# Kernel optimization log

Hardware: AMD Instinct MI355X
Metric: run time of the kernel (lower is better)

Reference implementation:

```python
import jax, jax.numpy as jnp
import numpy as np

D = 1024
H = 16
DH = D // H
FF = 4096
EPS = 1e-5


def _layernorm(x, g, b):
    m = jnp.mean(x, axis=-1, keepdims=True)
    v = jnp.mean(jnp.square(x - m), axis=-1, keepdims=True)
    return (x - m) * jax.lax.rsqrt(v + EPS) * g + b


def setup_inputs() -> dict:
    key = jax.random.key(0)
    ks = jax.random.split(key, 24)
    B, S = 2, 2048
    s = 0.02
    inp = {
        "tokens": jax.random.normal(ks[0], (B, S, D), jnp.float32),
        "attention_bias": jax.random.normal(ks[1], (B, S, S, 3), jnp.float32),
        "metadata_compatibility": jax.random.normal(ks[2], (B, S, S), jnp.float32),
        "key_padding_mask": jnp.zeros((B, S), jnp.bool_),
        "ln1_g": jnp.ones((D,), jnp.float32),
        "ln1_b": jnp.zeros((D,), jnp.float32),
        "Wq": jax.random.normal(ks[3], (D, D), jnp.float32) * s,
        "bq": jnp.zeros((D,), jnp.float32),
        "Wk": jax.random.normal(ks[4], (D, D), jnp.float32) * s,
        "bk": jnp.zeros((D,), jnp.float32),
        "Wv": jax.random.normal(ks[5], (D, D), jnp.float32) * s,
        "bv": jnp.zeros((D,), jnp.float32),
        "Wo": jax.random.normal(ks[6], (D, D), jnp.float32) * s,
        "bo": jnp.zeros((D,), jnp.float32),
        "Ws": jax.random.normal(ks[7], (3, H), jnp.float32) * s,
        "bs": jnp.zeros((H,), jnp.float32),
        "Wm": jax.random.normal(ks[8], (1, H), jnp.float32) * s,
        "bm": jnp.zeros((H,), jnp.float32),
        "ln2_g": jnp.ones((D,), jnp.float32),
        "ln2_b": jnp.zeros((D,), jnp.float32),
        "W1": jax.random.normal(ks[9], (D, FF), jnp.float32) * s,
        "b1": jnp.zeros((FF,), jnp.float32),
        "W2": jax.random.normal(ks[10], (FF, D), jnp.float32) * s,
        "b2": jnp.zeros((D,), jnp.float32),
    }
    return inp


def reference(tokens, attention_bias, metadata_compatibility, key_padding_mask,
              ln1_g, ln1_b, Wq, bq, Wk, bk, Wv, bv, Wo, bo,
              Ws, bs, Wm, bm, ln2_g, ln2_b, W1, b1, W2, b2):
    B, S, _ = tokens.shape
    scale = DH ** -0.5
    n = _layernorm(tokens, ln1_g, ln1_b)
    # project and split heads: [B,S,H,DH]
    q = (n @ Wq + bq).reshape(B, S, H, DH)
    k = (n @ Wk + bk).reshape(B, S, H, DH)
    v = (n @ Wv + bv).reshape(B, S, H, DH)
    logits = jnp.einsum('bihd,bjhd->bhij', q, k) * scale  # [B,H,S,S]
    # structural bias: Linear(3->H) then permute to [B,H,S,S]
    logits = logits + jnp.einsum('bijc,ch->bhij', attention_bias, Ws) + bs[None, :, None, None]
    # metadata bias: Linear(1->H)
    logits = logits + metadata_compatibility[:, None, :, :] * Wm[0][None, :, None, None] + bm[None, :, None, None]
    logits = jnp.where(key_padding_mask[:, None, None, :], -1e9, logits)
    w = jax.nn.softmax(logits, axis=-1)
    attended = jnp.einsum('bhij,bjhd->bihd', w, v).reshape(B, S, D)
    x = tokens + (attended @ Wo + bo)
    h = _layernorm(x, ln2_g, ln2_b)
    ff = jax.nn.gelu(h @ W1 + b1, approximate=False) @ W2 + b2
    return x + ff
```

## Files before the change

### kernel.cpp

```cpp
#include <hip/hip_runtime.h>

#define S_LEN 2048
#define DMODEL 1024
#define NH 16
#define DH 64
#define FFDIM 4096

typedef __bf16 bf16x8 __attribute__((ext_vector_type(8)));
typedef float f32x4 __attribute__((ext_vector_type(4)));
typedef unsigned short ushort_t;

#define AS1 __attribute__((address_space(1)))
#define AS3 __attribute__((address_space(3)))

__device__ __forceinline__ void gll16(const void* g, void* l) {
  __builtin_amdgcn_global_load_lds((AS1 const void*)g, (AS3 void*)l, 16, 0, 0);
}

__device__ __forceinline__ unsigned short f2b(float f){
  unsigned u = __builtin_bit_cast(unsigned, f);
  u = (u + 0x7FFFu + ((u >> 16) & 1u)) >> 16;
  return (unsigned short)u;
}

__device__ __forceinline__ float b2f(unsigned short us){
  return __builtin_bit_cast(float, (unsigned)us << 16);
}

__device__ __forceinline__ float gelu_exact(float x){
  return 0.5f * x * (1.0f + erff(x * 0.70710678118654752f));
}

__device__ __forceinline__ f32x4 mfma16(bf16x8 a, bf16x8 b, f32x4 c){
  return __builtin_amdgcn_mfma_f32_16x16x32_bf16(a, b, c, 0, 0, 0);
}

__global__ __launch_bounds__(256) void tconv_kernel(
    const float* __restrict__ W, ushort_t* __restrict__ Wt, int K, int N)
{
  __shared__ float tile[32][33];
  int tx = threadIdx.x, ty = threadIdx.y;
  int n0 = blockIdx.x * 32, k0 = blockIdx.y * 32;
#pragma unroll
  for (int i = 0; i < 4; ++i)
    tile[ty + i*8][tx] = W[(size_t)(k0 + ty + i*8) * N + n0 + tx];
  __syncthreads();
#pragma unroll
  for (int i = 0; i < 4; ++i)
    Wt[(size_t)(n0 + ty + i*8) * K + k0 + tx] = f2b(tile[tx][ty + i*8]);
}

__global__ __launch_bounds__(256) void ln_kernel(
    const float* __restrict__ x, const float* __restrict__ g,
    const float* __restrict__ bt, ushort_t* __restrict__ out)
{
  int row = blockIdx.x;
  int t = threadIdx.x;
  const float4 v = *(const float4*)&x[(size_t)row * DMODEL + t * 4];
  float s = v.x + v.y + v.z + v.w;
  float s2 = v.x*v.x + v.y*v.y + v.z*v.z + v.w*v.w;
#pragma unroll
  for (int d = 1; d < 64; d <<= 1) {
    s  += __shfl_xor(s,  d, 64);
    s2 += __shfl_xor(s2, d, 64);
  }
  __shared__ float red[8];
  int w = t >> 6;
  if ((t & 63) == 0) { red[w] = s; red[4 + w] = s2; }
  __syncthreads();
  s  = red[0] + red[1] + red[2] + red[3];
  s2 = red[4] + red[5] + red[6] + red[7];
  float mean = s * (1.0f / DMODEL);
  float var  = s2 * (1.0f / DMODEL) - mean * mean;
  float rstd = rsqrtf(var + 1e-5f);
  float4 gg = *(const float4*)&g[t * 4];
  float4 bb = *(const float4*)&bt[t * 4];
  ushort4 o;
  o.x = f2b((v.x - mean) * rstd * gg.x + bb.x);
  o.y = f2b((v.y - mean) * rstd * gg.y + bb.y);
  o.z = f2b((v.z - mean) * rstd * gg.z + bb.z);
  o.w = f2b((v.w - mean) * rstd * gg.w + bb.w);
  *(ushort4*)&out[(size_t)row * DMODEL + t * 4] = o;
}

__global__ __launch_bounds__(256) void bias_head_kernel(
    const float* __restrict__ ab, const float* __restrict__ mc,
    const unsigned char* __restrict__ kp,
    const float* __restrict__ Ws, const float* __restrict__ bs,
    const float* __restrict__ Wm, const float* __restrict__ bm,
    ushort_t* __restrict__ bp)
{
  int bi = blockIdx.x;
  int b = bi >> 11;
  int i = bi & (S_LEN - 1);
  int t = threadIdx.x;
  int j0 = t * 8;
  float av[24];
  const float4* A4 = (const float4*)(ab + ((size_t)bi * S_LEN + j0) * 3);
#pragma unroll
  for (int u = 0; u < 6; ++u) {
    float4 x = A4[u];
    av[u*4] = x.x; av[u*4+1] = x.y; av[u*4+2] = x.z; av[u*4+3] = x.w;
  }
  float mv[8];
  const float4* M4 = (const float4*)(mc + (size_t)bi * S_LEN + j0);
#pragma unroll
  for (int u = 0; u < 2; ++u) {
    float4 x = M4[u];
    mv[u*4] = x.x; mv[u*4+1] = x.y; mv[u*4+2] = x.z; mv[u*4+3] = x.w;
  }
  unsigned long long kq = *(const unsigned long long*)(kp + (size_t)b * S_LEN + j0);
#pragma unroll
  for (int h = 0; h < NH; ++h) {
    float w0 = Ws[h], w1 = Ws[NH + h], w2 = Ws[2*NH + h];
    float wm = Wm[h], cc = bs[h] + bm[h];
    alignas(16) ushort_t o[8];
#pragma unroll
    for (int j = 0; j < 8; ++j) {
      float v = av[j*3]*w0 + av[j*3+1]*w1 + av[j*3+2]*w2 + mv[j]*wm + cc;
      if ((kq >> (8*j)) & 1ull) v = -1e9f;
      o[j] = f2b(v);
    }
    *(uint4*)&bp[((size_t)(b*NH + h) * S_LEN + i) * S_LEN + j0] = *(const uint4*)o;
  }
}

__global__ __launch_bounds__(256) void bias_pack4_kernel(
    const float* __restrict__ ab, const float* __restrict__ mc,
    ushort_t* __restrict__ bp4)
{
  int bi = blockIdx.x;
  int t = threadIdx.x;
  int j0 = t * 8;
  const float4* A4 = (const float4*)(ab + ((size_t)bi * S_LEN + j0) * 3);
  float av[24];
#pragma unroll
  for (int u = 0; u < 6; ++u) {
    float4 x = A4[u];
    av[u*4] = x.x; av[u*4+1] = x.y; av[u*4+2] = x.z; av[u*4+3] = x.w;
  }
  float mv[8];
  const float4* M4 = (const float4*)(mc + (size_t)bi * S_LEN + j0);
#pragma unroll
  for (int u = 0; u < 2; ++u) {
    float4 x = M4[u];
    mv[u*4] = x.x; mv[u*4+1] = x.y; mv[u*4+2] = x.z; mv[u*4+3] = x.w;
  }
  alignas(16) ushort_t o[32];
#pragma unroll
  for (int j = 0; j < 8; ++j) {
    o[j*4]   = f2b(av[j*3]);
    o[j*4+1] = f2b(av[j*3+1]);
    o[j*4+2] = f2b(av[j*3+2]);
    o[j*4+3] = f2b(mv[j]);
  }
  uint4* dst = (uint4*)&bp4[((size_t)bi * S_LEN + j0) * 4];
#pragma unroll
  for (int u = 0; u < 4; ++u) dst[u] = ((const uint4*)o)[u];
}

template<int MODE>
__global__ __launch_bounds__(256) void gemm_bt(
    const ushort_t* __restrict__ A, const ushort_t* __restrict__ Bt,
    const float* __restrict__ b0p, const float* __restrict__ b1p,
    const float* __restrict__ b2p, const float* __restrict__ res,
    void* __restrict__ o0, void* __restrict__ o1, void* __restrict__ o2,
    int M, int N, int K)
{
  __shared__ ushort_t sh[8192];
  int t = threadIdx.x;
  int m0 = blockIdx.y * 128, n0 = blockIdx.x * 128;
  int w = t >> 6, l = t & 63, lr = l & 15, lg = l >> 4;
  int wr = (w >> 1) * 64, wc = (w & 1) * 64;

  const ushort_t* srcp[4];
  ushort_t* dstp[4];
#pragma unroll
  for (int j = 0; j < 4; ++j) {
    int c = j * 4 + w;
    int o = c * 1024 + l * 16;
    if (c < 8)
      srcp[j] = &A[(size_t)(m0 + (o >> 6)) * K + ((o & 63) >> 1)];
    else {
      int o2 = o - 8192;
      srcp[j] = &Bt[(size_t)(n0 + (o2 >> 6)) * K + ((o2 & 63) >> 1)];
    }
    dstp[j] = (ushort_t*)((char*)sh + o);
  }

  f32x4 acc[4][4] = {};
  for (int k0 = 0; k0 < K; k0 += 32) {
#pragma unroll
    for (int j = 0; j < 4; ++j) gll16(srcp[j] + k0, dstp[j]);
    __syncthreads();
    bf16x8 af[4], bfr[4];
#pragma unroll
    for (int a = 0; a < 4; ++a)
      af[a] = *(const bf16x8*)&sh[(wr + a * 16 + lr) * 32 + lg * 8];
#pragma unroll
    for (int b = 0; b < 4; ++b)
      bfr[b] = *(const bf16x8*)&sh[4096 + (wc + b * 16 + lr) * 32 + lg * 8];
#pragma unroll
    for (int a = 0; a < 4; ++a)
#pragma unroll
      for (int b = 0; b < 4; ++b)
        acc[a][b] = mfma16(af[a], bfr[b], acc[a][b]);
    __syncthreads();
  }

  if (MODE == 2) {
    float* out = (float*)o0;
#pragma unroll
    for (int a = 0; a < 4; ++a)
#pragma unroll
      for (int b = 0; b < 4; ++b) {
        int gn = n0 + wc + b * 16 + lr;
        float bv = b0p[gn];
#pragma unroll
        for (int r = 0; r < 4; ++r) {
          int gm = m0 + wr + a * 16 + lg * 4 + r;
          out[(size_t)gm * N + gn] = acc[a][b][r] + bv + res[(size_t)gm * N + gn];
        }
      }
  } else if (MODE == 3) {
    ushort_t* out = (ushort_t*)o0;
#pragma unroll
    for (int a = 0; a < 4; ++a)
#pragma unroll
      for (int b = 0; b < 4; ++b) {
        int gn = n0 + wc + b * 16 + lr;
        float bv = b0p[gn];
#pragma unroll
        for (int r = 0; r < 4; ++r) {
          int gm = m0 + wr + a * 16 + lg * 4 + r;
          out[(size_t)gm * N + gn] = f2b(gelu_exact(acc[a][b][r] + bv));
        }
      }
  } else {
    int seg = n0 >> 10;
    int nb0 = n0 & 1023;
    const float* bi = (seg == 0) ? b0p : (seg == 1) ? b1p : b2p;
    if (seg < 2) {
      ushort_t* out = (ushort_t*)((seg == 0) ? o0 : o1);
#pragma unroll
      for (int a = 0; a < 4; ++a)
#pragma unroll
        for (int b = 0; b < 4; ++b) {
          int nn = nb0 + wc + b * 16 + lr;
          float bv = bi[nn];
#pragma unroll
          for (int r = 0; r < 4; ++r) {
            int gm = m0 + wr + a * 16 + lg * 4 + r;
            out[(size_t)gm * DMODEL + nn] = f2b(acc[a][b][r] + bv);
          }
        }
    } else {
      ushort_t* out = (ushort_t*)o2;
#pragma unroll
      for (int a = 0; a < 4; ++a)
#pragma unroll
        for (int b = 0; b < 4; ++b) {
          int nn = nb0 + wc + b * 16 + lr;
          int gm = m0 + wr + a * 16 + lg * 4;
          float bv = bi[nn];
          ushort4 pk;
          pk.x = f2b(acc[a][b][0] + bv);
          pk.y = f2b(acc[a][b][1] + bv);
          pk.z = f2b(acc[a][b][2] + bv);
          pk.w = f2b(acc[a][b][3] + bv);
          size_t addr = (((size_t)(gm >> 11) * NH + (nn >> 6)) * DH + (nn & 63)) * S_LEN
                        + (gm & (S_LEN - 1));
          *(ushort4*)&out[addr] = pk;
        }
    }
  }
}

template<int BMODE>
__global__ __launch_bounds__(256) void attn_kernel(
    const ushort_t* __restrict__ q, const ushort_t* __restrict__ k,
    const ushort_t* __restrict__ vt,
    const ushort_t* __restrict__ bp,
    const float* __restrict__ ab, const float* __restrict__ mc,
    const unsigned char* __restrict__ kp,
    const float* __restrict__ Ws, const float* __restrict__ bs,
    const float* __restrict__ Wm, const float* __restrict__ bm,
    ushort_t* __restrict__ att)
{
  __shared__ ushort_t k_lds[64 * 80];
  __shared__ ushort_t v_lds[64 * 80];
  __shared__ ushort_t p_lds[4 * 16 * 80];
  int bh = blockIdx.y;
  int b = bh >> 4, h = bh & 15;
  int i0 = blockIdx.x * 64;
  int t = threadIdx.x, w = t >> 6, l = t & 63;
  int lr = l & 15, lg = l >> 4;
  float ws0 = 0, ws1 = 0, ws2 = 0, wmh = 0, cc = 0;
  if (BMODE != 0) {
    ws0 = Ws[h]; ws1 = Ws[NH + h]; ws2 = Ws[2 * NH + h];
    wmh = Wm[h]; cc = bs[h] + bm[h];
  }
  const float scale = 0.125f;

  int qrow = i0 + w * 16 + lr;
  size_t qbase = (size_t)(b * S_LEN + qrow) * DMODEL + h * DH;
  bf16x8 aq0 = *(const bf16x8*)&q[qbase + lg * 8];
  bf16x8 aq1 = *(const bf16x8*)&q[qbase + 32 + lg * 8];

  f32x4 acc_o[4] = {};
  float m_r[4], l_r[4];
#pragma unroll
  for (int r = 0; r < 4; ++r) { m_r[r] = -1e30f; l_r[r] = 0.0f; }

  for (int j0 = 0; j0 < S_LEN; j0 += 64) {
#pragma unroll
    for (int it = 0; it < 2; ++it) {
      int idx = t + it * 256;
      int row = idx >> 3, cg = idx & 7;
      *(uint4*)&k_lds[row * 80 + cg * 8] =
          *(const uint4*)&k[(size_t)(b * S_LEN + j0 + row) * DMODEL + h * DH + cg * 8];
      *(uint4*)&v_lds[row * 80 + cg * 8] =
          *(const uint4*)&vt[((size_t)(b * NH + h) * DH + row) * S_LEN + j0 + cg * 8];
    }
    __syncthreads();

    f32x4 acc_s[4] = {};
#pragma unroll
    for (int n = 0; n < 4; ++n) {
      bf16x8 b0 = *(const bf16x8*)&k_lds[(n * 16 + lr) * 80 + lg * 8];
      bf16x8 b1 = *(const bf16x8*)&k_lds[(n * 16 + lr) * 80 + 32 + lg * 8];
      acc_s[n] = mfma16(aq0, b0, acc_s[n]);
      acc_s[n] = mfma16(aq1, b1, acc_s[n]);
    }

    bool kpm[4] = {false, false, false, false};
    if (BMODE == 1 || BMODE == 2) {
#pragma unroll
      for (int n = 0; n < 4; ++n) kpm[n] = kp[b * S_LEN + j0 + n * 16 + lr];
    }

#pragma unroll
    for (int r = 0; r < 4; ++r) {
      int gr = i0 + w * 16 + lg * 4 + r;
      float pv[4];
      if (BMODE == 0) {
        size_t rb = ((size_t)bh * S_LEN + gr) * S_LEN + j0;
#pragma unroll
        for (int n = 0; n < 4; ++n) {
          float bv = b2f(bp[rb + n * 16 + lr]);
          pv[n] = fmaf(acc_s[n][r], scale, bv);
        }
      } else if (BMODE == 1) {
        size_t rb = ((size_t)(b * S_LEN + gr) * S_LEN + j0) * 4;
#pragma unroll
        for (int n = 0; n < 4; ++n) {
          const uint2 raw = *(const uint2*)&bp[rb + (size_t)(n * 16 + lr) * 4];
          float a0 = b2f((unsigned short)(raw.x & 0xFFFF));
          float a1 = b2f((unsigned short)(raw.x >> 16));
          float a2 = b2f((unsigned short)(raw.y & 0xFFFF));
          float mm = b2f((unsigned short)(raw.y >> 16));
          float v = fmaf(acc_s[n][r], scale,
                         a0 * ws0 + a1 * ws1 + a2 * ws2 + mm * wmh + cc);
          if (kpm[n]) v = -1e9f;
          pv[n] = v;
        }
      } else {
        size_t rb = (size_t)(b * S_LEN + gr) * S_LEN + j0;
#pragma unroll
        for (int n = 0; n < 4; ++n) {
          size_t base = rb + n * 16 + lr;
          float a0 = ab[base * 3], a1 = ab[base * 3 + 1], a2 = ab[base * 3 + 2];
          float mcv = mc[base];
          float v = fmaf(acc_s[n][r], scale,
                         a0 * ws0 + a1 * ws1 + a2 * ws2 + mcv * wmh + cc);
          if (kpm[n]) v = -1e9f;
          pv[n] = v;
        }
      }
      float mx = fmaxf(fmaxf(pv[0], pv[1]), fmaxf(pv[2], pv[3]));
#pragma unroll
      for (int d = 1; d < 16; d <<= 1) mx = fmaxf(mx, __shfl_xor(mx, d, 64));
      float mnew = fmaxf(m_r[r], mx);
      float sf = __expf(m_r[r] - mnew);
      float rs = 0.0f;
#pragma unroll
      for (int n = 0; n < 4; ++n) { pv[n] = __expf(pv[n] - mnew); rs += pv[n]; }
#pragma unroll
      for (int d = 1; d < 16; d <<= 1) rs += __shfl_xor(rs, d, 64);
      l_r[r] = l_r[r] * sf + rs;
      m_r[r] = mnew;
#pragma unroll
      for (int nd = 0; nd < 4; ++nd) acc_o[nd][r] *= sf;
#pragma unroll
      for (int n = 0; n < 4; ++n)
        p_lds[(w * 16 + lg * 4 + r) * 80 + n * 16 + lr] = f2b(pv[n]);
    }
    __syncthreads();

    bf16x8 ap0 = *(const bf16x8*)&p_lds[(w * 16 + lr) * 80 + lg * 8];
    bf16x8 ap1 = *(const bf16x8*)&p_lds[(w * 16 + lr) * 80 + 32 + lg * 8];
#pragma unroll
    for (int nd = 0; nd < 4; ++nd) {
      bf16x8 b0 = *(const bf16x8*)&v_lds[(nd * 16 + lr) * 80 + lg * 8];
      bf16x8 b1 = *(const bf16x8*)&v_lds[(nd * 16 + lr) * 80 + 32 + lg * 8];
      acc_o[nd] = mfma16(ap0, b0, acc_o[nd]);
      acc_o[nd] = mfma16(ap1, b1, acc_o[nd]);
    }
    __syncthreads();
  }

#pragma unroll
  for (int r = 0; r < 4; ++r) {
    int gr = i0 + w * 16 + lg * 4 + r;
    float inv = 1.0f / l_r[r];
#pragma unroll
    for (int nd = 0; nd < 4; ++nd)
      att[(size_t)(b * S_LEN + gr) * DMODEL + h * DH + nd * 16 + lr] =
          f2b(acc_o[nd][r] * inv);
  }
}

extern "C" void kernel_launch(void* const* d_in, const int* in_sizes, int n_in,
                              void* d_out, int out_size, void* d_ws, size_t ws_size,
                              hipStream_t stream) {
  const float* tokens = (const float*)d_in[0];
  const float* ab     = (const float*)d_in[1];
  const float* mc     = (const float*)d_in[2];
  const unsigned char* kp = (const unsigned char*)d_in[3];
  const float* ln1g = (const float*)d_in[4];
  const float* ln1b = (const float*)d_in[5];
  const float* Wq = (const float*)d_in[6];
  const float* bq = (const float*)d_in[7];
  const float* Wk = (const float*)d_in[8];
  const float* bk = (const float*)d_in[9];
  const float* Wv = (const float*)d_in[10];
  const float* bv = (const float*)d_in[11];
  const float* Wo = (const float*)d_in[12];
  const float* bo = (const float*)d_in[13];
  const float* Ws = (const float*)d_in[14];
  const float* bs = (const float*)d_in[15];
  const float* Wm = (const float*)d_in[16];
  const float* bm = (const float*)d_in[17];
  const float* ln2g = (const float*)d_in[18];
  const float* ln2b = (const float*)d_in[19];
  const float* W1 = (const float*)d_in[20];
  const float* b1 = (const float*)d_in[21];
  const float* W2 = (const float*)d_in[22];
  const float* b2 = (const float*)d_in[23];
  float* out = (float*)d_out;

  int B = in_sizes[0] / (S_LEN * DMODEL);
  int M = B * S_LEN;

  char* ws = (char*)d_ws;
  ushort_t* nb  = (ushort_t*)(ws + 0);
  ushort_t* qb  = (ushort_t*)(ws + (size_t)8388608);
  ushort_t* kb  = (ushort_t*)(ws + (size_t)16777216);
  ushort_t* vtb = (ushort_t*)(ws + (size_t)25165824);
  ushort_t* ff1 = (ushort_t*)(ws + 0);
  ushort_t* wt_q = (ushort_t*)(ws + (size_t)33554432);
  ushort_t* wt_k = (ushort_t*)(ws + (size_t)35651584);
  ushort_t* wt_v = (ushort_t*)(ws + (size_t)37748736);
  ushort_t* wt_o = (ushort_t*)(ws + (size_t)39845888);
  ushort_t* wt_1 = (ushort_t*)(ws + (size_t)41943040);
  ushort_t* wt_2 = (ushort_t*)(ws + (size_t)50331648);
  ushort_t* attb = (ushort_t*)(ws + (size_t)58720256);
  float*    xb   = (float*)   (ws + (size_t)67108864);
  ushort_t* hb   = (ushort_t*)(ws + (size_t)83886080);
  ushort_t* bp   = (ushort_t*)(ws + (size_t)92274688);

  size_t need_head  = 92274688ULL + (size_t)B * NH * S_LEN * S_LEN * 2;
  size_t need_pack4 = 92274688ULL + (size_t)B * S_LEN * S_LEN * 8;
  int bias_mode = (ws_size >= need_head) ? 0 : (ws_size >= need_pack4) ? 1 : 2;

  dim3 tb(32, 8);
  tconv_kernel<<<dim3(32, 32), tb, 0, stream>>>(Wq, wt_q, DMODEL, DMODEL);
  tconv_kernel<<<dim3(32, 32), tb, 0, stream>>>(Wk, wt_k, DMODEL, DMODEL);
  tconv_kernel<<<dim3(32, 32), tb, 0, stream>>>(Wv, wt_v, DMODEL, DMODEL);
  tconv_kernel<<<dim3(32, 32), tb, 0, stream>>>(Wo, wt_o, DMODEL, DMODEL);
  tconv_kernel<<<dim3(128, 32), tb, 0, stream>>>(W1, wt_1, DMODEL, FFDIM);
  tconv_kernel<<<dim3(32, 128), tb, 0, stream>>>(W2, wt_2, FFDIM, DMODEL);

  ln_kernel<<<M, 256, 0, stream>>>(tokens, ln1g, ln1b, nb);

  if (bias_mode == 0)
    bias_head_kernel<<<M, 256, 0, stream>>>(ab, mc, kp, Ws, bs, Wm, bm, bp);
  else if (bias_mode == 1)
    bias_pack4_kernel<<<M, 256, 0, stream>>>(ab, mc, bp);

  gemm_bt<4><<<dim3(24, M / 128), 256, 0, stream>>>(
      nb, wt_q, bq, bk, bv, nullptr, qb, kb, vtb, M, 3 * DMODEL, DMODEL);

  dim3 ag(S_LEN / 64, B * NH);
  if (bias_mode == 0)
    attn_kernel<0><<<ag, 256, 0, stream>>>(qb, kb, vtb, bp, ab, mc, kp,
                                           Ws, bs, Wm, bm, attb);
  else if (bias_mode == 1)
    attn_kernel<1><<<ag, 256, 0, stream>>>(qb, kb, vtb, bp, ab, mc, kp,
                                           Ws, bs, Wm, bm, attb);
  else
    attn_kernel<2><<<ag, 256, 0, stream>>>(qb, kb, vtb, nullptr, ab, mc, kp,
                                           Ws, bs, Wm, bm, attb);

  gemm_bt<2><<<dim3(8, M / 128), 256, 0, stream>>>(
      attb, wt_o, bo, nullptr, nullptr, tokens, xb, nullptr, nullptr,
      M, DMODEL, DMODEL);

  ln_kernel<<<M, 256, 0, stream>>>(xb, ln2g, ln2b, hb);

  gemm_bt<3><<<dim3(32, M / 128), 256, 0, stream>>>(
      hb, wt_1, b1, nullptr, nullptr, nullptr, ff1, nullptr, nullptr,
      M, FFDIM, DMODEL);

  gemm_bt<2><<<dim3(8, M / 128), 256, 0, stream>>>(
      ff1, wt_2, b2, nullptr, nullptr, xb, out, nullptr, nullptr,
      M, DMODEL, FFDIM);
}
```

Measured before the change: 758.7 us.

## Double-buffer GEMM and attention loads, fragment-order bias layout, fuse transposes

Several changes land together. The six weight-transpose launches become one kernel, and the GEMMs get double-buffered LDS staging with setprio around the MFMA blocks. The residual GEMMs move to a 128x64 tile kernel so more blocks launch. The bias is written in MFMA fragment order, so attention reads it with one vector load, and attention gets double-buffered, swizzled K/V staging through global_load_lds plus per-lane softmax. The fallback bias modes that depended on workspace size are removed, so the code now always assumes a large workspace.

```diff
diff --git a/kernel.cpp b/kernel.cpp
--- a/kernel.cpp
+++ b/kernel.cpp
@@ -27,6 +27,12 @@
   return __builtin_bit_cast(float, (unsigned)us << 16);
 }
 
+__device__ __forceinline__ unsigned cvt_pk_bf16(float lo, float hi){
+  unsigned r;
+  asm("v_cvt_pk_bf16_f32 %0, %1, %2" : "=v"(r) : "v"(lo), "v"(hi));
+  return r;
+}
+
 __device__ __forceinline__ float gelu_exact(float x){
   return 0.5f * x * (1.0f + erff(x * 0.70710678118654752f));
 }
@@ -35,12 +41,32 @@
   return __builtin_amdgcn_mfma_f32_16x16x32_bf16(a, b, c, 0, 0, 0);
 }
 
-__global__ __launch_bounds__(256) void tconv_kernel(
-    const float* __restrict__ W, ushort_t* __restrict__ Wt, int K, int N)
+__global__ __launch_bounds__(256) void tconv6(
+    const float* __restrict__ s0, const float* __restrict__ s1,
+    const float* __restrict__ s2, const float* __restrict__ s3,
+    const float* __restrict__ s4, const float* __restrict__ s5,
+    ushort_t* __restrict__ d0, ushort_t* __restrict__ d1,
+    ushort_t* __restrict__ d2, ushort_t* __restrict__ d3,
+    ushort_t* __restrict__ d4, ushort_t* __restrict__ d5)
 {
   __shared__ float tile[32][33];
+  int bx = blockIdx.x;
+  const float* W; ushort_t* Wt; int K, N, n0, k0;
+  if (bx < 4096) {
+    int seg = bx >> 10, t_ = bx & 1023;
+    W = (seg == 0) ? s0 : (seg == 1) ? s1 : (seg == 2) ? s2 : s3;
+    Wt = (seg == 0) ? d0 : (seg == 1) ? d1 : (seg == 2) ? d2 : d3;
+    K = 1024; N = 1024; n0 = (t_ & 31) * 32; k0 = (t_ >> 5) * 32;
+  } else if (bx < 8192) {
+    int t_ = bx - 4096;
+    W = s4; Wt = d4; K = 1024; N = 4096;
+    n0 = (t_ & 127) * 32; k0 = (t_ >> 7) * 32;
+  } else {
+    int t_ = bx - 8192;
+    W = s5; Wt = d5; K = 4096; N = 1024;
+    n0 = (t_ & 31) * 32; k0 = (t_ >> 5) * 32;
+  }
   int tx = threadIdx.x, ty = threadIdx.y;
-  int n0 = blockIdx.x * 32, k0 = blockIdx.y * 32;
 #pragma unroll
   for (int i = 0; i < 4; ++i)
     tile[ty + i*8][tx] = W[(size_t)(k0 + ty + i*8) * N + n0 + tx];
@@ -93,8 +119,13 @@
   int bi = blockIdx.x;
   int b = bi >> 11;
   int i = bi & (S_LEN - 1);
+  int qw = i >> 4, lr = i & 15;
   int t = threadIdx.x;
   int j0 = t * 8;
+  int jt = t >> 3;
+  int n  = (t & 7) >> 1;
+  int lg_a = ((t & 7) * 2) & 3;
+  int lg_b = lg_a + 1;
   float av[24];
   const float4* A4 = (const float4*)(ab + ((size_t)bi * S_LEN + j0) * 3);
 #pragma unroll
@@ -114,67 +145,38 @@
   for (int h = 0; h < NH; ++h) {
     float w0 = Ws[h], w1 = Ws[NH + h], w2 = Ws[2*NH + h];
     float wm = Wm[h], cc = bs[h] + bm[h];
-    alignas(16) ushort_t o[8];
+    float v[8];
 #pragma unroll
     for (int j = 0; j < 8; ++j) {
-      float v = av[j*3]*w0 + av[j*3+1]*w1 + av[j*3+2]*w2 + mv[j]*wm + cc;
-      if ((kq >> (8*j)) & 1ull) v = -1e9f;
-      o[j] = f2b(v);
-    }
-    *(uint4*)&bp[((size_t)(b*NH + h) * S_LEN + i) * S_LEN + j0] = *(const uint4*)o;
-  }
-}
-
-__global__ __launch_bounds__(256) void bias_pack4_kernel(
-    const float* __restrict__ ab, const float* __restrict__ mc,
-    ushort_t* __restrict__ bp4)
-{
-  int bi = blockIdx.x;
-  int t = threadIdx.x;
-  int j0 = t * 8;
-  const float4* A4 = (const float4*)(ab + ((size_t)bi * S_LEN + j0) * 3);
-  float av[24];
-#pragma unroll
-  for (int u = 0; u < 6; ++u) {
-    float4 x = A4[u];
-    av[u*4] = x.x; av[u*4+1] = x.y; av[u*4+2] = x.z; av[u*4+3] = x.w;
-  }
-  float mv[8];
-  const float4* M4 = (const float4*)(mc + (size_t)bi * S_LEN + j0);
-#pragma unroll
-  for (int u = 0; u < 2; ++u) {
-    float4 x = M4[u];
-    mv[u*4] = x.x; mv[u*4+1] = x.y; mv[u*4+2] = x.z; mv[u*4+3] = x.w;
-  }
-  alignas(16) ushort_t o[32];
-#pragma unroll
-  for (int j = 0; j < 8; ++j) {
-    o[j*4]   = f2b(av[j*3]);
-    o[j*4+1] = f2b(av[j*3+1]);
-    o[j*4+2] = f2b(av[j*3+2]);
-    o[j*4+3] = f2b(mv[j]);
-  }
-  uint4* dst = (uint4*)&bp4[((size_t)bi * S_LEN + j0) * 4];
-#pragma unroll
-  for (int u = 0; u < 4; ++u) dst[u] = ((const uint4*)o)[u];
+      float vv = av[j*3]*w0 + av[j*3+1]*w1 + av[j*3+2]*w2 + mv[j]*wm + cc;
+      if ((kq >> (8*j)) & 1ull) vv = -1e9f;
+      v[j] = vv;
+    }
+    size_t base = ((((size_t)(b*NH + h) * 32 + jt) * 128 + qw) * 4 + n) * 256;
+    uint2 u0, u1;
+    u0.x = cvt_pk_bf16(v[0], v[1]); u0.y = cvt_pk_bf16(v[2], v[3]);
+    u1.x = cvt_pk_bf16(v[4], v[5]); u1.y = cvt_pk_bf16(v[6], v[7]);
+    *(uint2*)&bp[base + (size_t)(lg_a*16 + lr) * 4] = u0;
+    *(uint2*)&bp[base + (size_t)(lg_b*16 + lr) * 4] = u1;
+  }
 }
 
 template<int MODE>
 __global__ __launch_bounds__(256) void gemm_bt(
     const ushort_t* __restrict__ A, const ushort_t* __restrict__ Bt,
     const float* __restrict__ b0p, const float* __restrict__ b1p,
-    const float* __restrict__ b2p, const float* __restrict__ res,
+    const float* __restrict__ b2p,
     void* __restrict__ o0, void* __restrict__ o1, void* __restrict__ o2,
     int M, int N, int K)
 {
-  __shared__ ushort_t sh[8192];
+  __shared__ ushort_t sh[2][8192];
   int t = threadIdx.x;
   int m0 = blockIdx.y * 128, n0 = blockIdx.x * 128;
   int w = t >> 6, l = t & 63, lr = l & 15, lg = l >> 4;
   int wr = (w >> 1) * 64, wc = (w & 1) * 64;
 
   const ushort_t* srcp[4];
-  ushort_t* dstp[4];
+  int dsto[4];
 #pragma unroll
   for (int j = 0; j < 4; ++j) {
     int c = j * 4 + w;
@@ -185,44 +187,41 @@
       int o2 = o - 8192;
       srcp[j] = &Bt[(size_t)(n0 + (o2 >> 6)) * K + ((o2 & 63) >> 1)];
     }
-    dstp[j] = (ushort_t*)((char*)sh + o);
-  }
-
+    dsto[j] = o;
+  }
+
+#define GSTAGE(bi, kk) do { \
+  _Pragma("unroll") \
+  for (int j = 0; j < 4; ++j) gll16(srcp[j] + (kk), (char*)sh[bi] + dsto[j]); \
+} while (0)
+
+  GSTAGE(0, 0);
+  __syncthreads();
   f32x4 acc[4][4] = {};
+  int cur = 0;
   for (int k0 = 0; k0 < K; k0 += 32) {
-#pragma unroll
-    for (int j = 0; j < 4; ++j) gll16(srcp[j] + k0, dstp[j]);
-    __syncthreads();
+    if (k0 + 32 < K) GSTAGE(cur ^ 1, k0 + 32);
+    const ushort_t* s = sh[cur];
     bf16x8 af[4], bfr[4];
 #pragma unroll
     for (int a = 0; a < 4; ++a)
-      af[a] = *(const bf16x8*)&sh[(wr + a * 16 + lr) * 32 + lg * 8];
+      af[a] = *(const bf16x8*)&s[(wr + a * 16 + lr) * 32 + lg * 8];
 #pragma unroll
     for (int b = 0; b < 4; ++b)
-      bfr[b] = *(const bf16x8*)&sh[4096 + (wc + b * 16 + lr) * 32 + lg * 8];
+      bfr[b] = *(const bf16x8*)&s[4096 + (wc + b * 16 + lr) * 32 + lg * 8];
+    __builtin_amdgcn_s_setprio(1);
 #pragma unroll
     for (int a = 0; a < 4; ++a)
 #pragma unroll
       for (int b = 0; b < 4; ++b)
         acc[a][b] = mfma16(af[a], bfr[b], acc[a][b]);
+    __builtin_amdgcn_s_setprio(0);
     __syncthreads();
-  }
-
-  if (MODE == 2) {
-    float* out = (float*)o0;
-#pragma unroll
-    for (int a = 0; a < 4; ++a)
-#pragma unroll
-      for (int b = 0; b < 4; ++b) {
-        int gn = n0 + wc + b * 16 + lr;
-        float bv = b0p[gn];
-#pragma unroll
-        for (int r = 0; r < 4; ++r) {
-          int gm = m0 + wr + a * 16 + lg * 4 + r;
-          out[(size_t)gm * N + gn] = acc[a][b][r] + bv + res[(size_t)gm * N + gn];
-        }
-      }
-  } else if (MODE == 3) {
+    cur ^= 1;
+  }
+#undef GSTAGE
+
+  if (MODE == 3) {
     ushort_t* out = (ushort_t*)o0;
 #pragma unroll
     for (int a = 0; a < 4; ++a)
@@ -276,147 +275,222 @@
   }
 }
 
-template<int BMODE>
+__global__ __launch_bounds__(256) void gemm64_res(
+    const ushort_t* __restrict__ A, const ushort_t* __restrict__ Bt,
+    const float* __restrict__ bias, const float* __restrict__ res,
+    float* __restrict__ out, int M, int N, int K)
+{
+  __shared__ ushort_t sh[2][6144];
+  int t = threadIdx.x;
+  int m0 = blockIdx.y * 128, n0 = blockIdx.x * 64;
+  int w = t >> 6, l = t & 63, lr = l & 15, lg = l >> 4;
+  int wr = (w >> 1) * 64, wc = (w & 1) * 32;
+
+  const ushort_t* srcp[3];
+  int dsto[3];
+#pragma unroll
+  for (int j = 0; j < 3; ++j) {
+    int c = j * 4 + w;
+    int o = c * 1024 + l * 16;
+    if (c < 8)
+      srcp[j] = &A[(size_t)(m0 + (o >> 6)) * K + ((o & 63) >> 1)];
+    else {
+      int o2 = o - 8192;
+      srcp[j] = &Bt[(size_t)(n0 + (o2 >> 6)) * K + ((o2 & 63) >> 1)];
+    }
+    dsto[j] = o;
+  }
+
+#define GSTAGE64(bi, kk) do { \
+  _Pragma("unroll") \
+  for (int j = 0; j < 3; ++j) gll16(srcp[j] + (kk), (char*)sh[bi] + dsto[j]); \
+} while (0)
+
+  GSTAGE64(0, 0);
+  __syncthreads();
+  f32x4 acc[4][2] = {};
+  int cur = 0;
+  for (int k0 = 0; k0 < K; k0 += 32) {
+    if (k0 + 32 < K) GSTAGE64(cur ^ 1, k0 + 32);
+    const ushort_t* s = sh[cur];
+    bf16x8 af[4], bfr[2];
+#pragma unroll
+    for (int a = 0; a < 4; ++a)
+      af[a] = *(const bf16x8*)&s[(wr + a * 16 + lr) * 32 + lg * 8];
+#pragma unroll
+    for (int b = 0; b < 2; ++b)
+      bfr[b] = *(const bf16x8*)&s[4096 + (wc + b * 16 + lr) * 32 + lg * 8];
+    __builtin_amdgcn_s_setprio(1);
+#pragma unroll
+    for (int a = 0; a < 4; ++a)
+#pragma unroll
+      for (int b = 0; b < 2; ++b)
+        acc[a][b] = mfma16(af[a], bfr[b], acc[a][b]);
+    __builtin_amdgcn_s_setprio(0);
+    __syncthreads();
+    cur ^= 1;
+  }
+#undef GSTAGE64
+
+#pragma unroll
+  for (int a = 0; a < 4; ++a)
+#pragma unroll
+    for (int b = 0; b < 2; ++b) {
+      int gn = n0 + wc + b * 16 + lr;
+      float bv = bias[gn];
+#pragma unroll
+      for (int r = 0; r < 4; ++r) {
+        int gm = m0 + wr + a * 16 + lg * 4 + r;
+        out[(size_t)gm * N + gn] = acc[a][b][r] + bv + res[(size_t)gm * N + gn];
+      }
+    }
+}
+
 __global__ __launch_bounds__(256) void attn_kernel(
     const ushort_t* __restrict__ q, const ushort_t* __restrict__ k,
-    const ushort_t* __restrict__ vt,
-    const ushort_t* __restrict__ bp,
-    const float* __restrict__ ab, const float* __restrict__ mc,
-    const unsigned char* __restrict__ kp,
-    const float* __restrict__ Ws, const float* __restrict__ bs,
-    const float* __restrict__ Wm, const float* __restrict__ bm,
+    const ushort_t* __restrict__ vt, const ushort_t* __restrict__ bp,
     ushort_t* __restrict__ att)
 {
-  __shared__ ushort_t k_lds[64 * 80];
-  __shared__ ushort_t v_lds[64 * 80];
-  __shared__ ushort_t p_lds[4 * 16 * 80];
+  __shared__ ushort_t kbuf[2][4096];
+  __shared__ ushort_t vbuf[2][4096];
+  __shared__ ushort_t p_lds[4096];
   int bh = blockIdx.y;
   int b = bh >> 4, h = bh & 15;
   int i0 = blockIdx.x * 64;
   int t = threadIdx.x, w = t >> 6, l = t & 63;
   int lr = l & 15, lg = l >> 4;
-  float ws0 = 0, ws1 = 0, ws2 = 0, wmh = 0, cc = 0;
-  if (BMODE != 0) {
-    ws0 = Ws[h]; ws1 = Ws[NH + h]; ws2 = Ws[2 * NH + h];
-    wmh = Wm[h]; cc = bs[h] + bm[h];
-  }
+  int rho = lr & 7;
   const float scale = 0.125f;
+
+  int srow0 = t >> 3, srow1 = 32 + (t >> 3);
+  int c16 = t & 7;
+  size_t kb0 = (size_t)b * S_LEN * DMODEL + h * DH;
+  size_t vb0 = (size_t)(b * NH + h) * DH * S_LEN;
+  size_t koff0 = (size_t)srow0 * DMODEL + ((c16 ^ (srow0 & 7)) << 3);
+  size_t koff1 = (size_t)srow1 * DMODEL + ((c16 ^ (srow1 & 7)) << 3);
+  size_t voff0 = (size_t)srow0 * S_LEN + ((c16 ^ (srow0 & 7)) << 3);
+  size_t voff1 = (size_t)srow1 * S_LEN + ((c16 ^ (srow1 & 7)) << 3);
+  int do0 = t * 8, do1 = 2048 + t * 8;
+
+#define STAGE_KV(bi, j0_) do { \
+  size_t kr = kb0 + (size_t)(j0_) * DMODEL; \
+  size_t vr = vb0 + (size_t)(j0_); \
+  gll16(k + kr + koff0, &kbuf[bi][do0]); \
+  gll16(k + kr + koff1, &kbuf[bi][do1]); \
+  gll16(vt + vr + voff0, &vbuf[bi][do0]); \
+  gll16(vt + vr + voff1, &vbuf[bi][do1]); \
+} while (0)
 
   int qrow = i0 + w * 16 + lr;
   size_t qbase = (size_t)(b * S_LEN + qrow) * DMODEL + h * DH;
   bf16x8 aq0 = *(const bf16x8*)&q[qbase + lg * 8];
   bf16x8 aq1 = *(const bf16x8*)&q[qbase + 32 + lg * 8];
 
+  int qw = blockIdx.x * 4 + w;
+  size_t fb0 = (((size_t)bh * 32) * 128 + qw) * 1024 + l * 4;
+
   f32x4 acc_o[4] = {};
-  float m_r[4], l_r[4];
-#pragma unroll
-  for (int r = 0; r < 4; ++r) { m_r[r] = -1e30f; l_r[r] = 0.0f; }
-
-  for (int j0 = 0; j0 < S_LEN; j0 += 64) {
-#pragma unroll
-    for (int it = 0; it < 2; ++it) {
-      int idx = t + it * 256;
-      int row = idx >> 3, cg = idx & 7;
-      *(uint4*)&k_lds[row * 80 + cg * 8] =
-          *(const uint4*)&k[(size_t)(b * S_LEN + j0 + row) * DMODEL + h * DH + cg * 8];
-      *(uint4*)&v_lds[row * 80 + cg * 8] =
-          *(const uint4*)&vt[((size_t)(b * NH + h) * DH + row) * S_LEN + j0 + cg * 8];
-    }
+  float m_run = -1e30f, l_run = 0.0f;
+
+  STAGE_KV(0, 0);
+  __syncthreads();
+
+  for (int jt = 0; jt < S_LEN / 64; ++jt) {
+    int cur = jt & 1;
+    if (jt + 1 < S_LEN / 64) STAGE_KV(cur ^ 1, (jt + 1) * 64);
+
+    const char* kbc = (const char*)kbuf[cur];
+    f32x4 acc_s[4] = {};
+    __builtin_amdgcn_s_setprio(1);
+#pragma unroll
+    for (int n = 0; n < 4; ++n) {
+      const char* rb = kbc + (n * 16 + lr) * 128;
+      bf16x8 k0 = *(const bf16x8*)(rb + ((lg ^ rho) << 4));
+      bf16x8 k1 = *(const bf16x8*)(rb + (((4 + lg) ^ rho) << 4));
+      acc_s[n] = mfma16(k0, aq0, acc_s[n]);
+      acc_s[n] = mfma16(k1, aq1, acc_s[n]);
+    }
+    __builtin_amdgcn_s_setprio(0);
+
+    float p[16];
+    size_t fb = fb0 + (size_t)jt * 131072;
+#pragma unroll
+    for (int n = 0; n < 4; ++n) {
+      uint2 raw = *(const uint2*)&bp[fb + n * 256];
+      p[n*4+0] = fmaf(acc_s[n][0], scale, b2f((unsigned short)(raw.x & 0xFFFF)));
+      p[n*4+1] = fmaf(acc_s[n][1], scale, b2f((unsigned short)(raw.x >> 16)));
+      p[n*4+2] = fmaf(acc_s[n][2], scale, b2f((unsigned short)(raw.y & 0xFFFF)));
+      p[n*4+3] = fmaf(acc_s[n][3], scale, b2f((unsigned short)(raw.y >> 16)));
+    }
+    float t8[8], t4[4];
+#pragma unroll
+    for (int i = 0; i < 8; ++i) t8[i] = fmaxf(p[i], p[i + 8]);
+#pragma unroll
+    for (int i = 0; i < 4; ++i) t4[i] = fmaxf(t8[i], t8[i + 4]);
+    float mx = fmaxf(fmaxf(t4[0], t4[1]), fmaxf(t4[2], t4[3]));
+    mx = fmaxf(mx, __shfl_xor(mx, 16, 64));
+    mx = fmaxf(mx, __shfl_xor(mx, 32, 64));
+    float mnew = fmaxf(m_run, mx);
+    float sf = __expf(m_run - mnew);
+    m_run = mnew;
+#pragma unroll
+    for (int i = 0; i < 16; ++i) p[i] = __expf(p[i] - mnew);
+    float s8[8], s4[4];
+#pragma unroll
+    for (int i = 0; i < 8; ++i) s8[i] = p[i] + p[i + 8];
+#pragma unroll
+    for (int i = 0; i < 4; ++i) s4[i] = s8[i] + s8[i + 4];
+    float ls = (s4[0] + s4[1]) + (s4[2] + s4[3]);
+    ls += __shfl_xor(ls, 16, 64);
+    ls += __shfl_xor(ls, 32, 64);
+    l_run = l_run * sf + ls;
+
+    float sfr[4];
+#pragma unroll
+    for (int r = 0; r < 4; ++r) sfr[r] = __shfl(sf, lg * 4 + r, 64);
+#pragma unroll
+    for (int nd = 0; nd < 4; ++nd)
+#pragma unroll
+      for (int r = 0; r < 4; ++r) acc_o[nd][r] *= sfr[r];
+
+    char* pb = (char*)p_lds + (w * 16 + lr) * 128;
+#pragma unroll
+    for (int n = 0; n < 4; ++n) {
+      uint2 pk2;
+      pk2.x = cvt_pk_bf16(p[n*4+0], p[n*4+1]);
+      pk2.y = cvt_pk_bf16(p[n*4+2], p[n*4+3]);
+      *(uint2*)(pb + ((n * 32 + lg * 8) ^ (rho << 4))) = pk2;
+    }
+    asm volatile("s_waitcnt lgkmcnt(0)" ::: "memory");
+    __builtin_amdgcn_sched_barrier(0);
+
+    bf16x8 ap0 = *(const bf16x8*)(pb + ((lg ^ rho) << 4));
+    bf16x8 ap1 = *(const bf16x8*)(pb + (((4 + lg) ^ rho) << 4));
+    const char* vbc = (const char*)vbuf[cur];
+    __builtin_amdgcn_s_setprio(1);
+#pragma unroll
+    for (int nd = 0; nd < 4; ++nd) {
+      const char* rb = vbc + (nd * 16 + lr) * 128;
+      bf16x8 v0 = *(const bf16x8*)(rb + ((lg ^ rho) << 4));
+      bf16x8 v1 = *(const bf16x8*)(rb + (((4 + lg) ^ rho) << 4));
+      acc_o[nd] = mfma16(ap0, v0, acc_o[nd]);
+      acc_o[nd] = mfma16(ap1, v1, acc_o[nd]);
+    }
+    __builtin_amdgcn_s_setprio(0);
     __syncthreads();
-
-    f32x4 acc_s[4] = {};
-#pragma unroll
-    for (int n = 0; n < 4; ++n) {
-      bf16x8 b0 = *(const bf16x8*)&k_lds[(n * 16 + lr) * 80 + lg * 8];
-      bf16x8 b1 = *(const bf16x8*)&k_lds[(n * 16 + lr) * 80 + 32 + lg * 8];
-      acc_s[n] = mfma16(aq0, b0, acc_s[n]);
-      acc_s[n] = mfma16(aq1, b1, acc_s[n]);
-    }
-
-    bool kpm[4] = {false, false, false, false};
-    if (BMODE == 1 || BMODE == 2) {
-#pragma unroll
-      for (int n = 0; n < 4; ++n) kpm[n] = kp[b * S_LEN + j0 + n * 16 + lr];
-    }
-
-#pragma unroll
-    for (int r = 0; r < 4; ++r) {
-      int gr = i0 + w * 16 + lg * 4 + r;
-      float pv[4];
-      if (BMODE == 0) {
-        size_t rb = ((size_t)bh * S_LEN + gr) * S_LEN + j0;
-#pragma unroll
-        for (int n = 0; n < 4; ++n) {
-          float bv = b2f(bp[rb + n * 16 + lr]);
-          pv[n] = fmaf(acc_s[n][r], scale, bv);
-        }
-      } else if (BMODE == 1) {
-        size_t rb = ((size_t)(b * S_LEN + gr) * S_LEN + j0) * 4;
-#pragma unroll
-        for (int n = 0; n < 4; ++n) {
-          const uint2 raw = *(const uint2*)&bp[rb + (size_t)(n * 16 + lr) * 4];
-          float a0 = b2f((unsigned short)(raw.x & 0xFFFF));
-          float a1 = b2f((unsigned short)(raw.x >> 16));
-          float a2 = b2f((unsigned short)(raw.y & 0xFFFF));
-          float mm = b2f((unsigned short)(raw.y >> 16));
-          float v = fmaf(acc_s[n][r], scale,
-                         a0 * ws0 + a1 * ws1 + a2 * ws2 + mm * wmh + cc);
-          if (kpm[n]) v = -1e9f;
-          pv[n] = v;
-        }
-      } else {
-        size_t rb = (size_t)(b * S_LEN + gr) * S_LEN + j0;
-#pragma unroll
-        for (int n = 0; n < 4; ++n) {
-          size_t base = rb + n * 16 + lr;
-          float a0 = ab[base * 3], a1 = ab[base * 3 + 1], a2 = ab[base * 3 + 2];
-          float mcv = mc[base];
-          float v = fmaf(acc_s[n][r], scale,
-                         a0 * ws0 + a1 * ws1 + a2 * ws2 + mcv * wmh + cc);
-          if (kpm[n]) v = -1e9f;
-          pv[n] = v;
-        }
-      }
-      float mx = fmaxf(fmaxf(pv[0], pv[1]), fmaxf(pv[2], pv[3]));
-#pragma unroll
-      for (int d = 1; d < 16; d <<= 1) mx = fmaxf(mx, __shfl_xor(mx, d, 64));
-      float mnew = fmaxf(m_r[r], mx);
-      float sf = __expf(m_r[r] - mnew);
-      float rs = 0.0f;
-#pragma unroll
-      for (int n = 0; n < 4; ++n) { pv[n] = __expf(pv[n] - mnew); rs += pv[n]; }
-#pragma unroll
-      for (int d = 1; d < 16; d <<= 1) rs += __shfl_xor(rs, d, 64);
-      l_r[r] = l_r[r] * sf + rs;
-      m_r[r] = mnew;
-#pragma unroll
-      for (int nd = 0; nd < 4; ++nd) acc_o[nd][r] *= sf;
-#pragma unroll
-      for (int n = 0; n < 4; ++n)
-        p_lds[(w * 16 + lg * 4 + r) * 80 + n * 16 + lr] = f2b(pv[n]);
-    }
-    __syncthreads();
-
-    bf16x8 ap0 = *(const bf16x8*)&p_lds[(w * 16 + lr) * 80 + lg * 8];
-    bf16x8 ap1 = *(const bf16x8*)&p_lds[(w * 16 + lr) * 80 + 32 + lg * 8];
-#pragma unroll
-    for (int nd = 0; nd < 4; ++nd) {
-      bf16x8 b0 = *(const bf16x8*)&v_lds[(nd * 16 + lr) * 80 + lg * 8];
-      bf16x8 b1 = *(const bf16x8*)&v_lds[(nd * 16 + lr) * 80 + 32 + lg * 8];
-      acc_o[nd] = mfma16(ap0, b0, acc_o[nd]);
-      acc_o[nd] = mfma16(ap1, b1, acc_o[nd]);
-    }
-    __syncthreads();
-  }
-
+  }
+#undef STAGE_KV
+
+  float inv[4];
+#pragma unroll
+  for (int r = 0; r < 4; ++r) inv[r] = 1.0f / __shfl(l_run, lg * 4 + r, 64);
 #pragma unroll
   for (int r = 0; r < 4; ++r) {
     int gr = i0 + w * 16 + lg * 4 + r;
-    float inv = 1.0f / l_r[r];
 #pragma unroll
     for (int nd = 0; nd < 4; ++nd)
       att[(size_t)(b * S_LEN + gr) * DMODEL + h * DH + nd * 16 + lr] =
-          f2b(acc_o[nd][r] * inv);
+          f2b(acc_o[nd][r] * inv[r]);
   }
 }
 
@@ -469,50 +543,26 @@
   ushort_t* hb   = (ushort_t*)(ws + (size_t)83886080);
   ushort_t* bp   = (ushort_t*)(ws + (size_t)92274688);
 
-  size_t need_head  = 92274688ULL + (size_t)B * NH * S_LEN * S_LEN * 2;
-  size_t need_pack4 = 92274688ULL + (size_t)B * S_LEN * S_LEN * 8;
-  int bias_mode = (ws_size >= need_head) ? 0 : (ws_size >= need_pack4) ? 1 : 2;
-
-  dim3 tb(32, 8);
-  tconv_kernel<<<dim3(32, 32), tb, 0, stream>>>(Wq, wt_q, DMODEL, DMODEL);
-  tconv_kernel<<<dim3(32, 32), tb, 0, stream>>>(Wk, wt_k, DMODEL, DMODEL);
-  tconv_kernel<<<dim3(32, 32), tb, 0, stream>>>(Wv, wt_v, DMODEL, DMODEL);
-  tconv_kernel<<<dim3(32, 32), tb, 0, stream>>>(Wo, wt_o, DMODEL, DMODEL);
-  tconv_kernel<<<dim3(128, 32), tb, 0, stream>>>(W1, wt_1, DMODEL, FFDIM);
-  tconv_kernel<<<dim3(32, 128), tb, 0, stream>>>(W2, wt_2, FFDIM, DMODEL);
+  tconv6<<<12288, dim3(32, 8), 0, stream>>>(Wq, Wk, Wv, Wo, W1, W2,
+                                            wt_q, wt_k, wt_v, wt_o, wt_1, wt_2);
 
   ln_kernel<<<M, 256, 0, stream>>>(tokens, ln1g, ln1b, nb);
 
-  if (bias_mode == 0)
-    bias_head_kernel<<<M, 256, 0, stream>>>(ab, mc, kp, Ws, bs, Wm, bm, bp);
-  else if (bias_mode == 1)
-    bias_pack4_kernel<<<M, 256, 0, stream>>>(ab, mc, bp);
+  bias_head_kernel<<<M, 256, 0, stream>>>(ab, mc, kp, Ws, bs, Wm, bm, bp);
 
   gemm_bt<4><<<dim3(24, M / 128), 256, 0, stream>>>(
-      nb, wt_q, bq, bk, bv, nullptr, qb, kb, vtb, M, 3 * DMODEL, DMODEL);
-
-  dim3 ag(S_LEN / 64, B * NH);
-  if (bias_mode == 0)
-    attn_kernel<0><<<ag, 256, 0, stream>>>(qb, kb, vtb, bp, ab, mc, kp,
-                                           Ws, bs, Wm, bm, attb);
-  else if (bias_mode == 1)
-    attn_kernel<1><<<ag, 256, 0, stream>>>(qb, kb, vtb, bp, ab, mc, kp,
-                                           Ws, bs, Wm, bm, attb);
-  else
-    attn_kernel<2><<<ag, 256, 0, stream>>>(qb, kb, vtb, nullptr, ab, mc, kp,
-                                           Ws, bs, Wm, bm, attb);
-
-  gemm_bt<2><<<dim3(8, M / 128), 256, 0, stream>>>(
-      attb, wt_o, bo, nullptr, nullptr, tokens, xb, nullptr, nullptr,
-      M, DMODEL, DMODEL);
+      nb, wt_q, bq, bk, bv, qb, kb, vtb, M, 3 * DMODEL, DMODEL);
+
+  attn_kernel<<<dim3(S_LEN / 64, B * NH), 256, 0, stream>>>(qb, kb, vtb, bp, attb);
+
+  gemm64_res<<<dim3(16, M / 128), 256, 0, stream>>>(
+      attb, wt_o, bo, tokens, xb, M, DMODEL, DMODEL);
 
   ln_kernel<<<M, 256, 0, stream>>>(xb, ln2g, ln2b, hb);
 
   gemm_bt<3><<<dim3(32, M / 128), 256, 0, stream>>>(
-      hb, wt_1, b1, nullptr, nullptr, nullptr, ff1, nullptr, nullptr,
-      M, FFDIM, DMODEL);
-
-  gemm_bt<2><<<dim3(8, M / 128), 256, 0, stream>>>(
-      ff1, wt_2, b2, nullptr, nullptr, xb, out, nullptr, nullptr,
-      M, DMODEL, FFDIM);
-}
+      hb, wt_1, b1, nullptr, nullptr, ff1, nullptr, nullptr, M, FFDIM, DMODEL);
+
+  gemm64_res<<<dim3(16, M / 128), 256, 0, stream>>>(
+      ff1, wt_2, b2, xb, out, M, DMODEL, FFDIM);
+}
```

Result: slower. 1.046 ms (+37.8%).
